# Kernel tuning notes

Hardware: AMD Instinct MI355X
Metric: run time of the kernel (lower is better)

## Reference

```python
import jax, jax.numpy as jnp
import numpy as np

B, T, X, H, N_LAYERS = 256, 128, 256, 1024, 3
W_STD = 0.01


def setup_inputs() -> dict:
    key = jax.random.key(0)
    ks = jax.random.split(key, 8)
    x = jax.random.normal(ks[0], (B, 1, X), dtype=jnp.float32)
    # fixed Euler time grid (torchdiffeq 'euler' steps exactly on these points)
    time_steps = jnp.arange(T, dtype=jnp.float32)
    W_in = W_STD * jax.random.normal(ks[1], (X, H), dtype=jnp.float32)
    b_in = W_STD * jax.random.normal(ks[2], (H,), dtype=jnp.float32)
    W_h = W_STD * jax.random.normal(ks[3], (N_LAYERS, H, H), dtype=jnp.float32)
    b_h = W_STD * jax.random.normal(ks[4], (N_LAYERS, H), dtype=jnp.float32)
    W_out = W_STD * jax.random.normal(ks[5], (H, X), dtype=jnp.float32)
    b_out = W_STD * jax.random.normal(ks[6], (X,), dtype=jnp.float32)
    return {"x": x, "time_steps": time_steps, "W_in": W_in, "b_in": b_in,
            "W_h": W_h, "b_h": b_h, "W_out": W_out, "b_out": b_out}


def _ode_func(y, W_in, b_in, W_h, b_h, W_out, b_out):
    # Linear -> [Tanh -> Linear]*n_layers -> Tanh -> Linear
    h = jnp.einsum('bix,xh->bih', y, W_in) + b_in
    for i in range(N_LAYERS):
        h = jnp.einsum('bih,hk->bik', jnp.tanh(h), W_h[i]) + b_h[i]
    return jnp.einsum('bih,hx->bix', jnp.tanh(h), W_out) + b_out


def reference(x, time_steps, W_in, b_in, W_h, b_h, W_out, b_out):
    dts = jnp.diff(time_steps)  # [T-1]

    def step(y, dt):
        y_next = y + dt * _ode_func(y, W_in, b_in, W_h, b_h, W_out, b_out)
        return y_next, y_next

    _, ys = jax.lax.scan(step, x, dts)            # [T-1, B, 1, X]
    full = jnp.concatenate([x[None], ys], axis=0)  # [T, B, 1, X]
    pred = jnp.transpose(full, (1, 0, 2, 3))[:, :, 0, :]  # [B, T, X]
    return pred
```

## Files before the change

kernel.cpp:

```cpp
#include <hip/hip_runtime.h>
#include <hip/hip_bf16.h>


typedef __attribute__((ext_vector_type(8))) short short8;
typedef __attribute__((ext_vector_type(4))) float f32x4;

#define AT_LD(p) __hip_atomic_load((p), __ATOMIC_RELAXED, __HIP_MEMORY_SCOPE_AGENT)
#define AT_ST(p, v) \
  __hip_atomic_store((p), (v), __ATOMIC_RELAXED, __HIP_MEMORY_SCOPE_AGENT)

#define GLD_BYPASS(dst, ptr) \
  asm volatile("global_load_dwordx4 %0, %1, off sc0 sc1" \
               : "=v"(dst) : "v"(ptr) : "memory")
#define VM_WAIT0()                                   \
  do {                                               \
    asm volatile("s_waitcnt vmcnt(0)" ::: "memory"); \
    __builtin_amdgcn_sched_barrier(0);               \
  } while (0)

__device__ inline unsigned short f2bf(float f) {
  unsigned u = __builtin_bit_cast(unsigned, f);
  unsigned r = u + 0x7FFFu + ((u >> 16) & 1u);
  return (unsigned short)(r >> 16);
}

__global__ __launch_bounds__(256, 1) void node_persistent(
    const float* __restrict__ x, const float* __restrict__ ts,
    const float* __restrict__ Win, const float* __restrict__ bin,
    const float* __restrict__ Wh, const float* __restrict__ bh,
    const float* __restrict__ Wout, const float* __restrict__ bout,
    float* __restrict__ out,
    unsigned* __restrict__ cnt,
    unsigned short* __restrict__ a0,
    unsigned short* __restrict__ a1) {
  alignas(16) __shared__ unsigned short sWh[3][16384];
  alignas(16) __shared__ unsigned short sWcomp[16384];
  alignas(16) __shared__ unsigned short sWin[4096];
  __shared__ float sBin[16], sBh[3][16], sBout[16], sBWc[16];
  __shared__ float sDt[128];

  const int bid = blockIdx.x;
  const int g = (bid & 7) >> 1;
  const int j = ((bid >> 3) << 1) | (bid & 1);
  const int tid = threadIdx.x;
  const int w = tid >> 6;
  const int l = tid & 63;
  const int lr = l & 15;
  const int lk = l >> 4;
  const int rowbase = g * 64 + w * 16;
  unsigned* slots = cnt + g * 64;

  for (int idx = tid; idx < 256 * 16; idx += 256) {
    int k = idx >> 4, c = idx & 15;
    sWin[((k >> 3) * 16 + c) * 8 + (k & 7)] = f2bf(Win[k * 1024 + j * 16 + c]);
  }
  for (int l3 = 0; l3 < 3; ++l3)
    for (int idx = tid; idx < 1024 * 16; idx += 256) {
      int k = idx >> 4, c = idx & 15;
      sWh[l3][((k >> 3) * 16 + c) * 8 + (k & 7)] =
          f2bf(Wh[(l3 * 1024 + k) * 1024 + j * 16 + c]);
    }
  if (tid < 16) {
    sBin[tid] = bin[j * 16 + tid];
    sBh[0][tid] = bh[j * 16 + tid];
    sBh[1][tid] = bh[1024 + j * 16 + tid];
    sBh[2][tid] = bh[2048 + j * 16 + tid];
    if (j < 16) sBout[tid] = bout[j * 16 + tid];
    float s = 0.f;
    for (int xx = 0; xx < 256; ++xx) s += bout[xx] * Win[xx * 1024 + j * 16 + tid];
    sBWc[tid] = s;
  }
  if (tid < 127) sDt[tid] = ts[tid + 1] - ts[tid];
  __syncthreads();

  for (int i = 0; i < 16; ++i) {
    int mt = w * 16 + i;
    f32x4 acc = {0.f, 0.f, 0.f, 0.f};
    const float* abase = Wout + (mt * 16 + lr) * 256 + lk * 8;
#pragma unroll
    for (int kk = 0; kk < 8; ++kk) {
      float4 f0 = *(const float4*)(abase + kk * 32);
      float4 f1 = *(const float4*)(abase + kk * 32 + 4);
      short8 a;
      a[0] = (short)f2bf(f0.x); a[1] = (short)f2bf(f0.y);
      a[2] = (short)f2bf(f0.z); a[3] = (short)f2bf(f0.w);
      a[4] = (short)f2bf(f1.x); a[5] = (short)f2bf(f1.y);
      a[6] = (short)f2bf(f1.z); a[7] = (short)f2bf(f1.w);
      short8 b = *(const short8*)(sWin + lk * 128 + lr * 8 + kk * 512);
      acc = __builtin_amdgcn_mfma_f32_16x16x32_bf16(a, b, acc, 0, 0, 0);
    }
#pragma unroll
    for (int r4 = 0; r4 < 4; ++r4) {
      int k = mt * 16 + lk * 4 + r4;
      sWcomp[((k >> 3) * 16 + lr) * 8 + (k & 7)] = f2bf(acc[r4]);
    }
  }

  unsigned short* a0g = a0 + (g << 16);
  unsigned short* a1g = a1 + (g << 16);
  const int colH = j * 16 + lr;
  const int pstore = (w << 14) + ((colH >> 5) << 9) + (((colH >> 3) & 3) << 7) +
                     (colH & 7);

  f32x4 u;
  {
    f32x4 acc = {0.f, 0.f, 0.f, 0.f};
    const float* xbase = x + (rowbase + lr) * 256 + lk * 8;
#pragma unroll
    for (int kk = 0; kk < 8; ++kk) {
      float4 f0 = *(const float4*)(xbase + kk * 32);
      float4 f1 = *(const float4*)(xbase + kk * 32 + 4);
      short8 a;
      a[0] = (short)f2bf(f0.x); a[1] = (short)f2bf(f0.y);
      a[2] = (short)f2bf(f0.z); a[3] = (short)f2bf(f0.w);
      a[4] = (short)f2bf(f1.x); a[5] = (short)f2bf(f1.y);
      a[6] = (short)f2bf(f1.z); a[7] = (short)f2bf(f1.w);
      short8 b = *(const short8*)(sWin + lk * 128 + lr * 8 + kk * 512);
      acc = __builtin_amdgcn_mfma_f32_16x16x32_bf16(a, b, acc, 0, 0, 0);
    }
#pragma unroll
    for (int r4 = 0; r4 < 4; ++r4) {
      u[r4] = acc[r4] + sBin[lr];
      AT_ST(&a0g[pstore + ((lk * 4 + r4) << 3)], f2bf(tanhf(u[r4])));
    }
  }

  f32x4 yreg = {0.f, 0.f, 0.f, 0.f};
  short8 wfrag[32];
  if (j < 16) {
    for (int idx = tid; idx < 64 * 16; idx += 256) {
      int r = idx >> 4, c = idx & 15;
      int row = g * 64 + r, col = j * 16 + c;
      out[(row * 128) * 256 + col] = x[row * 256 + col];
    }
#pragma unroll
    for (int r4 = 0; r4 < 4; ++r4)
      yreg[r4] = x[(rowbase + lk * 4 + r4) * 256 + j * 16 + lr];
#pragma unroll
    for (int kk = 0; kk < 32; ++kk) {
      short8 wv;
#pragma unroll
      for (int d = 0; d < 8; ++d)
        wv[d] = (short)f2bf(Wout[(lk * 8 + kk * 32 + d) * 256 + j * 16 + lr]);
      wfrag[kk] = wv;
    }
  }

  unsigned bn = 0;
  auto BAR = [&]() {
    ++bn;
    __syncthreads();
    if (tid < 64) {
      if (tid == 0) AT_ST(&slots[j], bn);
      for (;;) {
        unsigned v = AT_LD(&slots[tid]);
        if (__all((int)(v >= bn || tid == (unsigned)j))) break;
        __builtin_amdgcn_s_sleep(1);
      }
    }
    __syncthreads();
  };

  BAR();

  for (int t = 0; t < 127; ++t) {
    for (int l3 = 0; l3 < 3; ++l3) {
      const unsigned short* src = (l3 == 1) ? a1g : a0g;
      unsigned short* dst = (l3 == 1) ? a0g : a1g;
      const unsigned short* pb = src + (w << 14) + (l << 3);
      short8 af[32];
#pragma unroll
      for (int kk = 0; kk < 32; ++kk) GLD_BYPASS(af[kk], pb + (kk << 9));
      VM_WAIT0();
      f32x4 ac0 = {0.f, 0.f, 0.f, 0.f}, ac1 = {0.f, 0.f, 0.f, 0.f};
#pragma unroll
      for (int kk = 0; kk < 32; kk += 2) {
        short8 b0 = *(const short8*)(sWh[l3] + lk * 128 + lr * 8 + kk * 512);
        short8 b1 = *(const short8*)(sWh[l3] + lk * 128 + lr * 8 + (kk + 1) * 512);
        ac0 = __builtin_amdgcn_mfma_f32_16x16x32_bf16(af[kk], b0, ac0, 0, 0, 0);
        ac1 = __builtin_amdgcn_mfma_f32_16x16x32_bf16(af[kk + 1], b1, ac1, 0, 0, 0);
      }
      f32x4 acc = ac0 + ac1;
      float bias = sBh[l3][lr];
#pragma unroll
      for (int r4 = 0; r4 < 4; ++r4)
        AT_ST(&dst[pstore + ((lk * 4 + r4) << 3)], f2bf(tanhf(acc[r4] + bias)));
      BAR();
    }
    {
      float dt = sDt[t];
      const unsigned short* pb = a1g + (w << 14) + (l << 3);
      short8 af[32];
#pragma unroll
      for (int kk = 0; kk < 32; ++kk) GLD_BYPASS(af[kk], pb + (kk << 9));
      VM_WAIT0();
      f32x4 ac0 = {0.f, 0.f, 0.f, 0.f}, ac1 = {0.f, 0.f, 0.f, 0.f};
#pragma unroll
      for (int kk = 0; kk < 32; kk += 2) {
        short8 b0 = *(const short8*)(sWcomp + lk * 128 + lr * 8 + kk * 512);
        short8 b1 = *(const short8*)(sWcomp + lk * 128 + lr * 8 + (kk + 1) * 512);
        ac0 = __builtin_amdgcn_mfma_f32_16x16x32_bf16(af[kk], b0, ac0, 0, 0, 0);
        ac1 = __builtin_amdgcn_mfma_f32_16x16x32_bf16(af[kk + 1], b1, ac1, 0, 0, 0);
      }
      f32x4 accC = ac0 + ac1;
#pragma unroll
      for (int r4 = 0; r4 < 4; ++r4) {
        u[r4] += dt * (accC[r4] + sBWc[lr]);
        AT_ST(&a0g[pstore + ((lk * 4 + r4) << 3)], f2bf(tanhf(u[r4])));
      }
      if (j < 16) {
        f32x4 accO = {0.f, 0.f, 0.f, 0.f};
#pragma unroll
        for (int kk = 0; kk < 32; ++kk)
          accO = __builtin_amdgcn_mfma_f32_16x16x32_bf16(af[kk], wfrag[kk],
                                                         accO, 0, 0, 0);
#pragma unroll
        for (int r4 = 0; r4 < 4; ++r4) {
          float yv = yreg[r4] + dt * (accO[r4] + sBout[lr]);
          yreg[r4] = yv;
          int row = rowbase + lk * 4 + r4;
          out[(row * 128 + t + 1) * 256 + j * 16 + lr] = yv;
        }
      }
      BAR();
    }
  }
}

extern "C" void kernel_launch(void* const* d_in, const int* in_sizes, int n_in,
                              void* d_out, int out_size, void* d_ws, size_t ws_size,
                              hipStream_t stream) {
  (void)in_sizes; (void)n_in; (void)out_size; (void)ws_size;
  const float* x    = (const float*)d_in[0];
  const float* ts   = (const float*)d_in[1];
  const float* Win  = (const float*)d_in[2];
  const float* bin  = (const float*)d_in[3];
  const float* Wh   = (const float*)d_in[4];
  const float* bh   = (const float*)d_in[5];
  const float* Wout = (const float*)d_in[6];
  const float* bout = (const float*)d_in[7];
  float* out = (float*)d_out;

  char* ws = (char*)d_ws;
  unsigned* cnt = (unsigned*)ws;
  unsigned short* a0 = (unsigned short*)(ws + 4096);
  unsigned short* a1 = (unsigned short*)(ws + 4096 + 524288);

  hipMemsetAsync(ws, 0, 4096, stream);

  void* args[] = {(void*)&x,    (void*)&ts,  (void*)&Win,  (void*)&bin,
                  (void*)&Wh,   (void*)&bh,  (void*)&Wout, (void*)&bout,
                  (void*)&out,  (void*)&cnt, (void*)&a0,   (void*)&a1};
  hipError_t e = hipLaunchCooperativeKernel((const void*)node_persistent,
                                            dim3(256), dim3(256), args, 0, stream);
  if (e != hipSuccess) {
    hipLaunchKernelGGL(node_persistent, dim3(256), dim3(256), 0, stream,
                       x, ts, Win, bin, Wh, bh, Wout, bout, out, cnt, a0, a1);
  }
}
```

Before: 3.081 ms.

## Split hidden-layer GEMMs along K across four blocks with partial-sum exchange

```diff
diff --git a/kernel.cpp b/kernel.cpp
--- a/kernel.cpp
+++ b/kernel.cpp
@@ -9,22 +9,299 @@
 #define AT_ST(p, v) \
   __hip_atomic_store((p), (v), __ATOMIC_RELAXED, __HIP_MEMORY_SCOPE_AGENT)
 
-#define GLD_BYPASS(dst, ptr) \
+#define GLDX4(dst, ptr) \
   asm volatile("global_load_dwordx4 %0, %1, off sc0 sc1" \
                : "=v"(dst) : "v"(ptr) : "memory")
+#define GSTX4(ptr, val) \
+  asm volatile("global_store_dwordx4 %0, %1, off sc0 sc1" \
+               :: "v"(ptr), "v"(val) : "memory")
 #define VM_WAIT0()                                   \
   do {                                               \
     asm volatile("s_waitcnt vmcnt(0)" ::: "memory"); \
     __builtin_amdgcn_sched_barrier(0);               \
   } while (0)
 
+#define MFMA __builtin_amdgcn_mfma_f32_16x16x32_bf16
+
 __device__ inline unsigned short f2bf(float f) {
   unsigned u = __builtin_bit_cast(unsigned, f);
   unsigned r = u + 0x7FFFu + ((u >> 16) & 1u);
   return (unsigned short)(r >> 16);
 }
 
-__global__ __launch_bounds__(256, 1) void node_persistent(
+__global__ __launch_bounds__(256, 1) void node_ksplit(
+    const float* __restrict__ x, const float* __restrict__ ts,
+    const float* __restrict__ Win, const float* __restrict__ bin,
+    const float* __restrict__ Wh, const float* __restrict__ bh,
+    const float* __restrict__ Wout, const float* __restrict__ bout,
+    float* __restrict__ out,
+    unsigned* __restrict__ gslots, unsigned* __restrict__ sub,
+    float* __restrict__ pz,
+    unsigned short* __restrict__ a0, unsigned short* __restrict__ a1) {
+  alignas(16) __shared__ unsigned short sWh[3][16384];
+  alignas(16) __shared__ unsigned short sWcomp[16384];
+  __shared__ float sBh[3][16], sBWc[16], sBout[16], sDt[128];
+  __shared__ int s_dead;
+
+  const int bid = blockIdx.x;
+  const int g = bid >> 6;
+  const int loc = bid & 63;
+  const int s = loc >> 4;
+  const int n = loc & 15;
+  const int cg = n * 4 + s;
+  const int tid = threadIdx.x;
+  const int w = tid >> 6;
+  const int l = tid & 63;
+  const int lr = l & 15;
+  const int lk = l >> 4;
+  unsigned* myg = gslots + g * 64;
+  unsigned* mysub = sub + (g * 16 + n) * 4;
+
+  if (tid == 0) s_dead = 0;
+
+  unsigned short* wt = sWh[2];
+  for (int idx = tid; idx < 256 * 64; idx += 256) {
+    int k = idx >> 6, c = idx & 63;
+    wt[((k >> 3) * 64 + c) * 8 + (k & 7)] = f2bf(Win[k * 1024 + n * 64 + c]);
+  }
+  __syncthreads();
+
+  f32x4 u;
+  {
+    f32x4 acc = {0.f, 0.f, 0.f, 0.f};
+    const float* xb = x + (g * 64 + w * 16 + lr) * 256 + lk * 8;
+#pragma unroll
+    for (int kk = 0; kk < 8; ++kk) {
+      short8 a;
+#pragma unroll
+      for (int d = 0; d < 8; ++d) a[d] = (short)f2bf(xb[kk * 32 + d]);
+      short8 b = *(const short8*)(wt + kk * 2048 + lk * 512 + s * 128 + lr * 8);
+      acc = MFMA(a, b, acc, 0, 0, 0);
+    }
+#pragma unroll
+    for (int r4 = 0; r4 < 4; ++r4) u[r4] = acc[r4] + bin[cg * 16 + lr];
+  }
+
+  for (int i = 0; i < 4; ++i) {
+    int mt = w * 4 + i;
+    f32x4 c0 = {0,0,0,0}, c1 = {0,0,0,0}, c2 = {0,0,0,0}, c3 = {0,0,0,0};
+    const float* ab = Wout + (s * 256 + mt * 16 + lr) * 256 + lk * 8;
+#pragma unroll
+    for (int kk = 0; kk < 8; ++kk) {
+      short8 a;
+#pragma unroll
+      for (int d = 0; d < 8; ++d) a[d] = (short)f2bf(ab[kk * 32 + d]);
+      const unsigned short* bb = wt + kk * 2048 + lk * 512 + lr * 8;
+      c0 = MFMA(a, *(const short8*)(bb + 0),   c0, 0, 0, 0);
+      c1 = MFMA(a, *(const short8*)(bb + 128), c1, 0, 0, 0);
+      c2 = MFMA(a, *(const short8*)(bb + 256), c2, 0, 0, 0);
+      c3 = MFMA(a, *(const short8*)(bb + 384), c3, 0, 0, 0);
+    }
+    auto stc = [&](int nt, f32x4 a) {
+#pragma unroll
+      for (int r4 = 0; r4 < 4; ++r4) {
+        int kl = mt * 16 + lk * 4 + r4, cl = nt * 16 + lr;
+        sWcomp[((kl >> 3) * 64 + cl) * 8 + (kl & 7)] = f2bf(a[r4]);
+      }
+    };
+    stc(0, c0); stc(1, c1); stc(2, c2); stc(3, c3);
+  }
+  __syncthreads();
+
+  for (int m = 0; m < 3; ++m)
+    for (int idx = tid; idx < 256 * 64; idx += 256) {
+      int k = idx >> 6, c = idx & 63;
+      sWh[m][((k >> 3) * 64 + c) * 8 + (k & 7)] =
+          f2bf(Wh[(m * 1024 + s * 256 + k) * 1024 + n * 64 + c]);
+    }
+  if (tid < 16) {
+    sBh[0][tid] = bh[cg * 16 + tid];
+    sBh[1][tid] = bh[1024 + cg * 16 + tid];
+    sBh[2][tid] = bh[2048 + cg * 16 + tid];
+    sBout[tid] = bout[n * 16 + tid];
+    float sum = 0.f;
+    for (int xx = 0; xx < 256; ++xx)
+      sum += bout[xx] * Win[xx * 1024 + cg * 16 + tid];
+    sBWc[tid] = sum;
+  }
+  if (tid < 127) sDt[tid] = ts[tid + 1] - ts[tid];
+
+  unsigned short* a0g = a0 + (g << 16);
+  unsigned short* a1g = a1 + (g << 16);
+  const int ccol = cg * 16 + lr;
+  const int pcol = ((ccol >> 5) << 9) + (((ccol >> 3) & 3) << 7) + (ccol & 7);
+#pragma unroll
+  for (int r4 = 0; r4 < 4; ++r4)
+    AT_ST(&a0g[(w << 14) + pcol + ((lk * 4 + r4) << 3)], f2bf(tanhf(u[r4])));
+
+  f32x4 yreg = {0.f, 0.f, 0.f, 0.f};
+  short8 wfrag[32];
+  if (s == 0) {
+    for (int idx = tid; idx < 64 * 16; idx += 256) {
+      int r = idx >> 4, c = idx & 15;
+      out[((g * 64 + r) * 128) * 256 + n * 16 + c] =
+          x[(g * 64 + r) * 256 + n * 16 + c];
+    }
+#pragma unroll
+    for (int r4 = 0; r4 < 4; ++r4)
+      yreg[r4] = x[(g * 64 + w * 16 + lk * 4 + r4) * 256 + n * 16 + lr];
+#pragma unroll
+    for (int kk = 0; kk < 32; ++kk) {
+      short8 wv;
+#pragma unroll
+      for (int d = 0; d < 8; ++d)
+        wv[d] = (short)f2bf(Wout[(lk * 8 + kk * 32 + d) * 256 + n * 16 + lr]);
+      wfrag[kk] = wv;
+    }
+  }
+
+  unsigned ph = 0;
+  auto BAR = [&]() {
+    VM_WAIT0();
+    __syncthreads();
+    if (!s_dead) {
+      if (tid < 64) {
+        if (tid == 0) AT_ST(&myg[loc], ph);
+        int it = 0;
+        for (;;) {
+          unsigned v = AT_LD(&myg[tid]);
+          if (__all((int)(v >= ph || tid == loc))) break;
+          if (++it > (1 << 20)) { if (tid == 0) s_dead = 1; break; }
+          __builtin_amdgcn_s_sleep(1);
+        }
+      }
+    }
+    __syncthreads();
+  };
+  auto SUBBAR = [&]() {
+    VM_WAIT0();
+    __syncthreads();
+    if (!s_dead) {
+      if (tid < 4) {
+        if (tid == 0) AT_ST(&mysub[s], ph);
+        int it = 0;
+        for (;;) {
+          unsigned v = AT_LD(&mysub[tid]);
+          if (__all((int)(v >= ph || tid == s))) break;
+          if (++it > (1 << 20)) { if (tid == 0) s_dead = 1; break; }
+          __builtin_amdgcn_s_sleep(1);
+        }
+      }
+    }
+    __syncthreads();
+  };
+
+  ++ph;
+  BAR();
+
+  const int toff = lr * 64 + w * 16 + lk * 4;
+  float* pzb = pz + ((g * 16 + n) << 14);
+
+  for (int t = 0; t < 127; ++t) {
+    for (int l3 = 0; l3 < 3; ++l3) {
+      const unsigned short* src = (l3 & 1) ? a1g : a0g;
+      unsigned short* dst = (l3 & 1) ? a0g : a1g;
+      ++ph;
+      const unsigned short* pb = src + (w << 14) + (s << 12) + (l << 3);
+      short8 af[8];
+#pragma unroll
+      for (int kk = 0; kk < 8; ++kk) GLDX4(af[kk], pb + (kk << 9));
+      VM_WAIT0();
+      f32x4 q0 = {0,0,0,0}, q1 = {0,0,0,0}, q2 = {0,0,0,0}, q3 = {0,0,0,0};
+#pragma unroll
+      for (int kk = 0; kk < 8; ++kk) {
+        const unsigned short* bb = sWh[l3] + kk * 2048 + lk * 512 + lr * 8;
+        q0 = MFMA(af[kk], *(const short8*)(bb + 0),   q0, 0, 0, 0);
+        q1 = MFMA(af[kk], *(const short8*)(bb + 128), q1, 0, 0, 0);
+        q2 = MFMA(af[kk], *(const short8*)(bb + 256), q2, 0, 0, 0);
+        q3 = MFMA(af[kk], *(const short8*)(bb + 384), q3, 0, 0, 0);
+      }
+      float* sbase = pzb + (s << 12) + toff;
+      if (s != 0) GSTX4(sbase + 0 * 1024, q0);
+      if (s != 1) GSTX4(sbase + 1 * 1024, q1);
+      if (s != 2) GSTX4(sbase + 2 * 1024, q2);
+      if (s != 3) GSTX4(sbase + 3 * 1024, q3);
+      SUBBAR();
+      f32x4 own = (s == 0) ? q0 : (s == 1) ? q1 : (s == 2) ? q2 : q3;
+      const float* rb = pzb + (s << 10) + toff;
+      f32x4 r0 = {0,0,0,0}, r1 = {0,0,0,0}, r2 = {0,0,0,0}, r3 = {0,0,0,0};
+      if (s != 0) GLDX4(r0, rb + (0 << 12));
+      if (s != 1) GLDX4(r1, rb + (1 << 12));
+      if (s != 2) GLDX4(r2, rb + (2 << 12));
+      if (s != 3) GLDX4(r3, rb + (3 << 12));
+      VM_WAIT0();
+      f32x4 sum = r0 + r1 + r2 + r3 + own;
+      float bias = sBh[l3][lr];
+#pragma unroll
+      for (int r4 = 0; r4 < 4; ++r4)
+        AT_ST(&dst[(w << 14) + pcol + ((lk * 4 + r4) << 3)],
+              f2bf(tanhf(sum[r4] + bias)));
+      BAR();
+    }
+    {
+      ++ph;
+      float dt = sDt[t];
+      short8 af[32];
+      f32x4 accO = {0.f, 0.f, 0.f, 0.f};
+      if (s == 0) {
+        const unsigned short* pbf = a1g + (w << 14) + (l << 3);
+#pragma unroll
+        for (int kk = 0; kk < 32; ++kk) GLDX4(af[kk], pbf + (kk << 9));
+        VM_WAIT0();
+#pragma unroll
+        for (int kk = 0; kk < 32; ++kk)
+          accO = MFMA(af[kk], wfrag[kk], accO, 0, 0, 0);
+      } else {
+        const unsigned short* pb = a1g + (w << 14) + (s << 12) + (l << 3);
+#pragma unroll
+        for (int kk = 0; kk < 8; ++kk) GLDX4(af[kk], pb + (kk << 9));
+        VM_WAIT0();
+      }
+      f32x4 q0 = {0,0,0,0}, q1 = {0,0,0,0}, q2 = {0,0,0,0}, q3 = {0,0,0,0};
+#pragma unroll
+      for (int kk = 0; kk < 8; ++kk) {
+        const unsigned short* bb = sWcomp + kk * 2048 + lk * 512 + lr * 8;
+        q0 = MFMA(af[kk], *(const short8*)(bb + 0),   q0, 0, 0, 0);
+        q1 = MFMA(af[kk], *(const short8*)(bb + 128), q1, 0, 0, 0);
+        q2 = MFMA(af[kk], *(const short8*)(bb + 256), q2, 0, 0, 0);
+        q3 = MFMA(af[kk], *(const short8*)(bb + 384), q3, 0, 0, 0);
+      }
+      float* sbase = pzb + (s << 12) + toff;
+      if (s != 0) GSTX4(sbase + 0 * 1024, q0);
+      if (s != 1) GSTX4(sbase + 1 * 1024, q1);
+      if (s != 2) GSTX4(sbase + 2 * 1024, q2);
+      if (s != 3) GSTX4(sbase + 3 * 1024, q3);
+      SUBBAR();
+      f32x4 own = (s == 0) ? q0 : (s == 1) ? q1 : (s == 2) ? q2 : q3;
+      const float* rb = pzb + (s << 10) + toff;
+      f32x4 r0 = {0,0,0,0}, r1 = {0,0,0,0}, r2 = {0,0,0,0}, r3 = {0,0,0,0};
+      if (s != 0) GLDX4(r0, rb + (0 << 12));
+      if (s != 1) GLDX4(r1, rb + (1 << 12));
+      if (s != 2) GLDX4(r2, rb + (2 << 12));
+      if (s != 3) GLDX4(r3, rb + (3 << 12));
+      VM_WAIT0();
+      f32x4 sum = r0 + r1 + r2 + r3 + own;
+#pragma unroll
+      for (int r4 = 0; r4 < 4; ++r4) {
+        u[r4] += dt * (sum[r4] + sBWc[lr]);
+        AT_ST(&a0g[(w << 14) + pcol + ((lk * 4 + r4) << 3)],
+              f2bf(tanhf(u[r4])));
+      }
+      if (s == 0) {
+#pragma unroll
+        for (int r4 = 0; r4 < 4; ++r4) {
+          float yv = yreg[r4] + dt * (accO[r4] + sBout[lr]);
+          yreg[r4] = yv;
+          out[((g * 64 + w * 16 + lk * 4 + r4) * 128 + t + 1) * 256 + n * 16 +
+              lr] = yv;
+        }
+      }
+      BAR();
+    }
+  }
+}
+
+__global__ __launch_bounds__(256, 1) void node_r5(
     const float* __restrict__ x, const float* __restrict__ ts,
     const float* __restrict__ Win, const float* __restrict__ bin,
     const float* __restrict__ Wh, const float* __restrict__ bh,
@@ -87,7 +364,7 @@
       a[4] = (short)f2bf(f1.x); a[5] = (short)f2bf(f1.y);
       a[6] = (short)f2bf(f1.z); a[7] = (short)f2bf(f1.w);
       short8 b = *(const short8*)(sWin + lk * 128 + lr * 8 + kk * 512);
-      acc = __builtin_amdgcn_mfma_f32_16x16x32_bf16(a, b, acc, 0, 0, 0);
+      acc = MFMA(a, b, acc, 0, 0, 0);
     }
 #pragma unroll
     for (int r4 = 0; r4 < 4; ++r4) {
@@ -116,7 +393,7 @@
       a[4] = (short)f2bf(f1.x); a[5] = (short)f2bf(f1.y);
       a[6] = (short)f2bf(f1.z); a[7] = (short)f2bf(f1.w);
       short8 b = *(const short8*)(sWin + lk * 128 + lr * 8 + kk * 512);
-      acc = __builtin_amdgcn_mfma_f32_16x16x32_bf16(a, b, acc, 0, 0, 0);
+      acc = MFMA(a, b, acc, 0, 0, 0);
     }
 #pragma unroll
     for (int r4 = 0; r4 < 4; ++r4) {
@@ -170,15 +447,15 @@
       const unsigned short* pb = src + (w << 14) + (l << 3);
       short8 af[32];
 #pragma unroll
-      for (int kk = 0; kk < 32; ++kk) GLD_BYPASS(af[kk], pb + (kk << 9));
+      for (int kk = 0; kk < 32; ++kk) GLDX4(af[kk], pb + (kk << 9));
       VM_WAIT0();
       f32x4 ac0 = {0.f, 0.f, 0.f, 0.f}, ac1 = {0.f, 0.f, 0.f, 0.f};
 #pragma unroll
       for (int kk = 0; kk < 32; kk += 2) {
         short8 b0 = *(const short8*)(sWh[l3] + lk * 128 + lr * 8 + kk * 512);
         short8 b1 = *(const short8*)(sWh[l3] + lk * 128 + lr * 8 + (kk + 1) * 512);
-        ac0 = __builtin_amdgcn_mfma_f32_16x16x32_bf16(af[kk], b0, ac0, 0, 0, 0);
-        ac1 = __builtin_amdgcn_mfma_f32_16x16x32_bf16(af[kk + 1], b1, ac1, 0, 0, 0);
+        ac0 = MFMA(af[kk], b0, ac0, 0, 0, 0);
+        ac1 = MFMA(af[kk + 1], b1, ac1, 0, 0, 0);
       }
       f32x4 acc = ac0 + ac1;
       float bias = sBh[l3][lr];
@@ -192,15 +469,15 @@
       const unsigned short* pb = a1g + (w << 14) + (l << 3);
       short8 af[32];
 #pragma unroll
-      for (int kk = 0; kk < 32; ++kk) GLD_BYPASS(af[kk], pb + (kk << 9));
+      for (int kk = 0; kk < 32; ++kk) GLDX4(af[kk], pb + (kk << 9));
       VM_WAIT0();
       f32x4 ac0 = {0.f, 0.f, 0.f, 0.f}, ac1 = {0.f, 0.f, 0.f, 0.f};
 #pragma unroll
       for (int kk = 0; kk < 32; kk += 2) {
         short8 b0 = *(const short8*)(sWcomp + lk * 128 + lr * 8 + kk * 512);
         short8 b1 = *(const short8*)(sWcomp + lk * 128 + lr * 8 + (kk + 1) * 512);
-        ac0 = __builtin_amdgcn_mfma_f32_16x16x32_bf16(af[kk], b0, ac0, 0, 0, 0);
-        ac1 = __builtin_amdgcn_mfma_f32_16x16x32_bf16(af[kk + 1], b1, ac1, 0, 0, 0);
+        ac0 = MFMA(af[kk], b0, ac0, 0, 0, 0);
+        ac1 = MFMA(af[kk + 1], b1, ac1, 0, 0, 0);
       }
       f32x4 accC = ac0 + ac1;
 #pragma unroll
@@ -212,8 +489,7 @@
         f32x4 accO = {0.f, 0.f, 0.f, 0.f};
 #pragma unroll
         for (int kk = 0; kk < 32; ++kk)
-          accO = __builtin_amdgcn_mfma_f32_16x16x32_bf16(af[kk], wfrag[kk],
-                                                         accO, 0, 0, 0);
+          accO = MFMA(af[kk], wfrag[kk], accO, 0, 0, 0);
 #pragma unroll
         for (int r4 = 0; r4 < 4; ++r4) {
           float yv = yreg[r4] + dt * (accO[r4] + sBout[lr]);
@@ -230,7 +506,7 @@
 extern "C" void kernel_launch(void* const* d_in, const int* in_sizes, int n_in,
                               void* d_out, int out_size, void* d_ws, size_t ws_size,
                               hipStream_t stream) {
-  (void)in_sizes; (void)n_in; (void)out_size; (void)ws_size;
+  (void)in_sizes; (void)n_in; (void)out_size;
   const float* x    = (const float*)d_in[0];
   const float* ts   = (const float*)d_in[1];
   const float* Win  = (const float*)d_in[2];
@@ -242,19 +518,39 @@
   float* out = (float*)d_out;
 
   char* ws = (char*)d_ws;
-  unsigned* cnt = (unsigned*)ws;
+  unsigned* gslots = (unsigned*)ws;
+  unsigned* sub    = (unsigned*)(ws + 2048);
   unsigned short* a0 = (unsigned short*)(ws + 4096);
   unsigned short* a1 = (unsigned short*)(ws + 4096 + 524288);
+  float* pz = (float*)(ws + 4096 + 1048576);
 
   hipMemsetAsync(ws, 0, 4096, stream);
 
-  void* args[] = {(void*)&x,    (void*)&ts,  (void*)&Win,  (void*)&bin,
-                  (void*)&Wh,   (void*)&bh,  (void*)&Wout, (void*)&bout,
-                  (void*)&out,  (void*)&cnt, (void*)&a0,   (void*)&a1};
-  hipError_t e = hipLaunchCooperativeKernel((const void*)node_persistent,
-                                            dim3(256), dim3(256), args, 0, stream);
-  if (e != hipSuccess) {
-    hipLaunchKernelGGL(node_persistent, dim3(256), dim3(256), 0, stream,
-                       x, ts, Win, bin, Wh, bh, Wout, bout, out, cnt, a0, a1);
+  const size_t need_v2 = 4096 + 1048576 + 4194304;
+  if (ws_size >= need_v2 + (1 << 20)) {
+    void* args[] = {(void*)&x,   (void*)&ts,     (void*)&Win,  (void*)&bin,
+                    (void*)&Wh,  (void*)&bh,     (void*)&Wout, (void*)&bout,
+                    (void*)&out, (void*)&gslots, (void*)&sub,  (void*)&pz,
+                    (void*)&a0,  (void*)&a1};
+    hipError_t e = hipLaunchCooperativeKernel((const void*)node_ksplit,
+                                              dim3(256), dim3(256), args, 0,
+                                              stream);
+    if (e != hipSuccess) {
+      hipLaunchKernelGGL(node_ksplit, dim3(256), dim3(256), 0, stream,
+                         x, ts, Win, bin, Wh, bh, Wout, bout, out, gslots, sub,
+                         pz, a0, a1);
+    }
+  } else {
+    void* args[] = {(void*)&x,    (void*)&ts,     (void*)&Win,  (void*)&bin,
+                    (void*)&Wh,   (void*)&bh,     (void*)&Wout, (void*)&bout,
+                    (void*)&out,  (void*)&gslots, (void*)&a0,   (void*)&a1};
+    hipError_t e = hipLaunchCooperativeKernel((const void*)node_r5,
+                                              dim3(256), dim3(256), args, 0,
+                                              stream);
+    if (e != hipSuccess) {
+      hipLaunchKernelGGL(node_r5, dim3(256), dim3(256), 0, stream,
+                         x, ts, Win, bin, Wh, bh, Wout, bout, out, gslots, a0,
+                         a1);
+    }
   }
 }
```

Result: slower. 4.590 ms (+49.0%).
